# Kernel optimization log

Hardware: AMD Instinct MI355X
Metric: run time of the kernel (lower is better)

Reference implementation:

```python
import jax, jax.numpy as jnp
import numpy as np

N_NODES = 50000
N_EDGES = 800000
F_IN = 128
HID = 128
N_GRAPHS = 512


def setup_inputs() -> dict:
    key = jax.random.key(0)
    k0, k1, k2, k3, k4 = jax.random.split(key, 5)
    x = jax.random.normal(k0, (N_NODES, F_IN), dtype=jnp.float32)
    edge_index = jax.random.randint(k1, (2, N_EDGES), 0, N_NODES)
    batch = jnp.sort(jax.random.randint(k2, (N_NODES,), 0, N_GRAPHS))
    W1 = jax.random.normal(k3, (F_IN, HID), dtype=jnp.float32) / np.sqrt(F_IN).astype(np.float32)
    b1 = jnp.zeros((HID,), dtype=jnp.float32)
    W2 = jax.random.normal(k4, (HID, HID), dtype=jnp.float32) / np.sqrt(HID).astype(np.float32)
    b2 = jnp.zeros((HID,), dtype=jnp.float32)
    return {"x": x, "W1": W1, "b1": b1, "W2": W2, "b2": b2,
            "edge_index": edge_index, "batch": batch}


def _gcn_conv(x, W, b, src, dst, norm, n_nodes):
    # PyG GCNConv: linear transform, then D^-1/2 (A+I) D^-1/2 aggregation, then bias
    h = x @ W                              # [N, H]
    msg = h[src] * norm[:, None]           # gather + edgewise scale  [E+N, H]
    out = jax.ops.segment_sum(msg, dst, num_segments=n_nodes)  # scatter-add
    return out + b


def reference(x, W1, b1, W2, b2, edge_index, batch):
    n = x.shape[0]
    loops = jnp.arange(n)
    src = jnp.concatenate([edge_index[0], loops])   # add self-loops
    dst = jnp.concatenate([edge_index[1], loops])
    deg = jax.ops.segment_sum(jnp.ones_like(dst, dtype=x.dtype), dst, num_segments=n)
    dinv = jax.lax.rsqrt(deg)                       # deg >= 1 due to self-loops
    norm = dinv[src] * dinv[dst]

    h = jax.nn.relu(_gcn_conv(x, W1, b1, src, dst, norm, n))
    h = jax.nn.relu(_gcn_conv(h, W2, b2, src, dst, norm, n))

    # readout mode 'all': concat(add, max, mean) pooling over graphs
    s = jax.ops.segment_sum(h, batch, num_segments=N_GRAPHS)        # [G, H]
    cnt = jax.ops.segment_sum(jnp.ones((n, 1), h.dtype), batch, num_segments=N_GRAPHS)
    mean = s / jnp.maximum(cnt, 1.0)
    mx = jax.ops.segment_max(h, batch, num_segments=N_GRAPHS)
    mx = jnp.where(cnt > 0, mx, 0.0)                # guard empty graphs
    # dropout(p=0.2) is identity in eval mode
    return jnp.concatenate([s, mx, mean], axis=1)   # [G, 3*H]
```

## Files before the change

kernel.cpp:

```cpp
#include <hip/hip_runtime.h>

#define N_NODES 50000
#define N_EDGES 800000
#define FEAT 128
#define N_GRAPHS 512

#define SCAN_BLK 256
#define N_SCAN_BLOCKS ((N_NODES + SCAN_BLK - 1) / SCAN_BLK)

__device__ __forceinline__ unsigned int f2bf(float f) {
    unsigned int u = __float_as_uint(f);
    return (u + 0x7fffu + ((u >> 16) & 1u)) >> 16;
}
__device__ __forceinline__ float bf_lo(unsigned int u) { return __uint_as_float(u << 16); }
__device__ __forceinline__ float bf_hi(unsigned int u) { return __uint_as_float(u & 0xffff0000u); }

__global__ __launch_bounds__(256) void count_kernel(const int* __restrict__ dst,
                                                    int* __restrict__ cnt) {
    int e = blockIdx.x * 256 + threadIdx.x;
    if (e < N_EDGES) atomicAdd(&cnt[__builtin_nontemporal_load(dst + e)], 1);
}

__global__ __launch_bounds__(SCAN_BLK) void scan_partial_kernel(const int* __restrict__ cnt,
                                                                int* __restrict__ partial) {
    __shared__ int s[SCAN_BLK];
    int i = blockIdx.x * SCAN_BLK + threadIdx.x;
    s[threadIdx.x] = (i < N_NODES) ? cnt[i] : 0;
    __syncthreads();
#pragma unroll
    for (int off = SCAN_BLK / 2; off > 0; off >>= 1) {
        if (threadIdx.x < off) s[threadIdx.x] += s[threadIdx.x + off];
        __syncthreads();
    }
    if (threadIdx.x == 0) partial[blockIdx.x] = s[0];
}

__global__ __launch_bounds__(SCAN_BLK) void scan_apply_kernel(const int* __restrict__ cnt,
                                                              const int* __restrict__ partial,
                                                              int* __restrict__ rowptr,
                                                              float* __restrict__ dinv) {
    __shared__ int s[SCAN_BLK];
    __shared__ int sbase;
    int t = threadIdx.x;
    int bid = blockIdx.x;

    s[t] = (t < bid) ? partial[t] : 0;
    __syncthreads();
#pragma unroll
    for (int off = SCAN_BLK / 2; off > 0; off >>= 1) {
        if (t < off) s[t] += s[t + off];
        __syncthreads();
    }
    if (t == 0) sbase = s[0];
    __syncthreads();

    int i = bid * SCAN_BLK + t;
    int v = (i < N_NODES) ? cnt[i] : 0;
    s[t] = v;
    __syncthreads();
#pragma unroll
    for (int off = 1; off < SCAN_BLK; off <<= 1) {
        int u = (t >= off) ? s[t - off] : 0;
        __syncthreads();
        s[t] += u;
        __syncthreads();
    }
    if (i < N_NODES) {
        rowptr[i] = sbase + s[t] - v;
        dinv[i] = rsqrtf((float)(v + 1));
    }
    if (bid == 0 && t == 0) rowptr[N_NODES] = N_EDGES;
}

__global__ __launch_bounds__(256) void scatter_kernel(const int* __restrict__ src,
                                                      const int* __restrict__ dst,
                                                      const int* __restrict__ rowptr,
                                                      int* __restrict__ woff,
                                                      unsigned short* __restrict__ csr_src) {
    int e = blockIdx.x * 256 + threadIdx.x;
    if (e >= N_EDGES) return;
    int s = __builtin_nontemporal_load(src + e);
    int d = __builtin_nontemporal_load(dst + e);
    int pos = atomicAdd(&woff[d], 1);
    csr_src[rowptr[d] + pos] = (unsigned short)s;
}

__global__ __launch_bounds__(256) void gemm_kernel(const float* __restrict__ X,
                                                   const float* __restrict__ W,
                                                   const float* __restrict__ dinv,
                                                   unsigned int* __restrict__ G, int M) {
    __shared__ float sX[64][132];
    __shared__ float sW[64][132];
    int tid = threadIdx.x;
    int row0 = blockIdx.x * 64;

#pragma unroll
    for (int it = 0; it < 8; ++it) {
        int idx = tid + it * 256;
        int r = idx >> 5, q = idx & 31;
        int grow = row0 + r;
        float4 v = make_float4(0.f, 0.f, 0.f, 0.f);
        if (grow < M) v = *reinterpret_cast<const float4*>(X + grow * 128 + q * 4);
        *reinterpret_cast<float4*>(&sX[r][q * 4]) = v;
    }

    int tx = tid & 15;
    int ty = tid >> 4;
    float acc[4][8];
#pragma unroll
    for (int i = 0; i < 4; ++i)
#pragma unroll
        for (int j = 0; j < 8; ++j) acc[i][j] = 0.f;

    for (int k0 = 0; k0 < 128; k0 += 64) {
        __syncthreads();
#pragma unroll
        for (int it = 0; it < 8; ++it) {
            int idx = tid + it * 256;
            int r = idx >> 5, q = idx & 31;
            *reinterpret_cast<float4*>(&sW[r][q * 4]) =
                *reinterpret_cast<const float4*>(W + (k0 + r) * 128 + q * 4);
        }
        __syncthreads();
#pragma unroll 16
        for (int k = 0; k < 64; ++k) {
            float xv[4];
#pragma unroll
            for (int ri = 0; ri < 4; ++ri) xv[ri] = sX[ty * 4 + ri][k0 + k];
            float4 w0 = *reinterpret_cast<const float4*>(&sW[k][tx * 4]);
            float4 w1 = *reinterpret_cast<const float4*>(&sW[k][64 + tx * 4]);
            float wv[8] = {w0.x, w0.y, w0.z, w0.w, w1.x, w1.y, w1.z, w1.w};
#pragma unroll
            for (int ri = 0; ri < 4; ++ri)
#pragma unroll
                for (int ci = 0; ci < 8; ++ci) acc[ri][ci] += xv[ri] * wv[ci];
        }
    }
#pragma unroll
    for (int ri = 0; ri < 4; ++ri) {
        int grow = row0 + ty * 4 + ri;
        if (grow >= M) continue;
        float sc = dinv[grow];
        uint2 lo, hi;
        lo.x = f2bf(sc * acc[ri][0]) | (f2bf(sc * acc[ri][1]) << 16);
        lo.y = f2bf(sc * acc[ri][2]) | (f2bf(sc * acc[ri][3]) << 16);
        hi.x = f2bf(sc * acc[ri][4]) | (f2bf(sc * acc[ri][5]) << 16);
        hi.y = f2bf(sc * acc[ri][6]) | (f2bf(sc * acc[ri][7]) << 16);
        *reinterpret_cast<uint2*>(G + grow * 64 + tx * 2) = lo;
        *reinterpret_cast<uint2*>(G + grow * 64 + 32 + tx * 2) = hi;
    }
}

__global__ __launch_bounds__(256) void aggregate_kernel(const uint4* __restrict__ G4,
                                                        const float* __restrict__ dinv,
                                                        const int* __restrict__ rowptr,
                                                        const unsigned short* __restrict__ csr_src,
                                                        const float* __restrict__ bias,
                                                        float* __restrict__ Hout, int n) {
    int tid = threadIdx.x;
    int node = blockIdx.x * 16 + (tid >> 4);
    int lane16 = tid & 15;
    bool active = node < n;

    int start = active ? rowptr[node] : 0;
    int end = active ? rowptr[node + 1] : 0;

    float a[8] = {0.f, 0.f, 0.f, 0.f, 0.f, 0.f, 0.f, 0.f};
    if (active) {
        uint4 u = G4[node * 16 + lane16];
        a[0] += bf_lo(u.x); a[1] += bf_hi(u.x);
        a[2] += bf_lo(u.y); a[3] += bf_hi(u.y);
        a[4] += bf_lo(u.z); a[5] += bf_hi(u.z);
        a[6] += bf_lo(u.w); a[7] += bf_hi(u.w);
    }

#define ACC_ROW(sidx)                                   \
    {                                                   \
        uint4 u = G4[(sidx) * 16 + lane16];             \
        a[0] += bf_lo(u.x); a[1] += bf_hi(u.x);         \
        a[2] += bf_lo(u.y); a[3] += bf_hi(u.y);         \
        a[4] += bf_lo(u.z); a[5] += bf_hi(u.z);         \
        a[6] += bf_lo(u.w); a[7] += bf_hi(u.w);         \
    }

    for (int base = start; base < end; base += 16) {
        int idx = base + lane16;
        int s_l = (idx < end) ? (int)csr_src[idx] : 0;
        int nn = min(16, end - base);
        if (nn == 16) {
#pragma unroll 8
            for (int j = 0; j < 16; ++j) {
                int s = __shfl(s_l, j, 16);
                ACC_ROW(s);
            }
        } else {
#pragma unroll 4
            for (int j = 0; j < nn; ++j) {
                int s = __shfl(s_l, j, 16);
                ACC_ROW(s);
            }
        }
    }
#undef ACC_ROW

    if (active) {
        float di = dinv[node];
        float4 b0 = *reinterpret_cast<const float4*>(bias + lane16 * 8);
        float4 b1 = *reinterpret_cast<const float4*>(bias + lane16 * 8 + 4);
        float4 o0, o1;
        o0.x = fmaxf(di * a[0] + b0.x, 0.f);
        o0.y = fmaxf(di * a[1] + b0.y, 0.f);
        o0.z = fmaxf(di * a[2] + b0.z, 0.f);
        o0.w = fmaxf(di * a[3] + b0.w, 0.f);
        o1.x = fmaxf(di * a[4] + b1.x, 0.f);
        o1.y = fmaxf(di * a[5] + b1.y, 0.f);
        o1.z = fmaxf(di * a[6] + b1.z, 0.f);
        o1.w = fmaxf(di * a[7] + b1.w, 0.f);
        *reinterpret_cast<float4*>(Hout + node * 128 + lane16 * 8) = o0;
        *reinterpret_cast<float4*>(Hout + node * 128 + lane16 * 8 + 4) = o1;
    }
}

__global__ __launch_bounds__(256) void readout_kernel(const float* __restrict__ H,
                                                      const int* __restrict__ batch,
                                                      float* __restrict__ out) {
    int g = blockIdx.x;
    int f = threadIdx.x & 127;
    int half = threadIdx.x >> 7;
    const int n = N_NODES;
    auto lb = [&](int key) {
        int lo = 0, hi = n;
        while (lo < hi) {
            int mid = (lo + hi) >> 1;
            if (batch[mid] < key) lo = mid + 1; else hi = mid;
        }
        return lo;
    };
    int start = lb(g), end = lb(g + 1);
    float sum = 0.f, mx = 0.f;
    for (int i = start + half; i < end; i += 2) {
        float v = H[i * 128 + f];
        sum += v;
        mx = fmaxf(mx, v);
    }
    __shared__ float ssum[256], smax[256];
    ssum[threadIdx.x] = sum;
    smax[threadIdx.x] = mx;
    __syncthreads();
    if (half == 0) {
        sum += ssum[threadIdx.x + 128];
        mx = fmaxf(mx, smax[threadIdx.x + 128]);
        int cntg = end - start;
        float mean = sum / fmaxf((float)cntg, 1.0f);
        out[g * 384 + f] = sum;
        out[g * 384 + 128 + f] = mx;
        out[g * 384 + 256 + f] = mean;
    }
}

extern "C" void kernel_launch(void* const* d_in, const int* in_sizes, int n_in,
                              void* d_out, int out_size, void* d_ws, size_t ws_size,
                              hipStream_t stream) {
    const float* x = (const float*)d_in[0];
    const float* W1 = (const float*)d_in[1];
    const float* b1 = (const float*)d_in[2];
    const float* W2 = (const float*)d_in[3];
    const float* b2 = (const float*)d_in[4];
    const int* ei = (const int*)d_in[5];
    const int* batch = (const int*)d_in[6];
    const int* esrc = ei;
    const int* edst = ei + N_EDGES;
    float* out = (float*)d_out;

    char* ws = (char*)d_ws;
    int* cnt       = (int*)(ws + 0);
    int* woff      = (int*)(ws + 200704);
    int* rowptr    = (int*)(ws + 401408);
    float* dinv    = (float*)(ws + 602112);
    int* partial   = (int*)(ws + 802816);
    unsigned short* csr_src = (unsigned short*)(ws + 804864);
    unsigned int* bufG = (unsigned int*)(ws + 2404864);
    float* bufH    = (float*)(ws + 15204864);

    hipMemsetAsync(cnt, 0, N_NODES * sizeof(int), stream);
    hipMemsetAsync(woff, 0, N_NODES * sizeof(int), stream);

    count_kernel<<<N_EDGES / 256, 256, 0, stream>>>(edst, cnt);
    scan_partial_kernel<<<N_SCAN_BLOCKS, SCAN_BLK, 0, stream>>>(cnt, partial);
    scan_apply_kernel<<<N_SCAN_BLOCKS, SCAN_BLK, 0, stream>>>(cnt, partial, rowptr, dinv);
    scatter_kernel<<<N_EDGES / 256, 256, 0, stream>>>(esrc, edst, rowptr, woff, csr_src);

    int gemm_blocks = (N_NODES + 63) / 64;
    int agg_blocks = (N_NODES + 15) / 16;
    gemm_kernel<<<gemm_blocks, 256, 0, stream>>>(x, W1, dinv, bufG, N_NODES);
    aggregate_kernel<<<agg_blocks, 256, 0, stream>>>((const uint4*)bufG, dinv, rowptr, csr_src, b1, bufH, N_NODES);
    gemm_kernel<<<gemm_blocks, 256, 0, stream>>>(bufH, W2, dinv, bufG, N_NODES);
    aggregate_kernel<<<agg_blocks, 256, 0, stream>>>((const uint4*)bufG, dinv, rowptr, csr_src, b2, bufH, N_NODES);
    readout_kernel<<<N_GRAPHS, 256, 0, stream>>>(bufH, batch, out);
}
```

Baseline: 334.2 us.

## Use bf16 MFMA for node-feature GEMM with pre-transposed bf16 weights

After: 330.8 us. Within noise of the previous version (-1.0%).

```diff
diff --git a/kernel.cpp b/kernel.cpp
--- a/kernel.cpp
+++ b/kernel.cpp
@@ -7,6 +7,10 @@
 
 #define SCAN_BLK 256
 #define N_SCAN_BLOCKS ((N_NODES + SCAN_BLK - 1) / SCAN_BLK)
+#define LDK 136
+
+typedef __attribute__((ext_vector_type(8))) short short8;
+typedef __attribute__((ext_vector_type(4))) float f32x4;
 
 __device__ __forceinline__ unsigned int f2bf(float f) {
     unsigned int u = __float_as_uint(f);
@@ -85,12 +89,23 @@
     csr_src[rowptr[d] + pos] = (unsigned short)s;
 }
 
+__global__ __launch_bounds__(256) void wt_kernel(const float* __restrict__ W,
+                                                 unsigned short* __restrict__ Wt) {
+    int t = threadIdx.x;
+#pragma unroll
+    for (int i = 0; i < 64; ++i) {
+        int idx = t + 256 * i;
+        int k = idx >> 7, n = idx & 127;
+        Wt[n * 128 + k] = (unsigned short)f2bf(W[idx]);
+    }
+}
+
 __global__ __launch_bounds__(256) void gemm_kernel(const float* __restrict__ X,
-                                                   const float* __restrict__ W,
+                                                   const unsigned short* __restrict__ Wt,
                                                    const float* __restrict__ dinv,
-                                                   unsigned int* __restrict__ G, int M) {
-    __shared__ float sX[64][132];
-    __shared__ float sW[64][132];
+                                                   unsigned short* __restrict__ G16, int M) {
+    __shared__ unsigned short sX[64][LDK];
+    __shared__ unsigned short sW[128][LDK];
     int tid = threadIdx.x;
     int row0 = blockIdx.x * 64;
 
@@ -101,53 +116,51 @@
         int grow = row0 + r;
         float4 v = make_float4(0.f, 0.f, 0.f, 0.f);
         if (grow < M) v = *reinterpret_cast<const float4*>(X + grow * 128 + q * 4);
-        *reinterpret_cast<float4*>(&sX[r][q * 4]) = v;
-    }
-
-    int tx = tid & 15;
-    int ty = tid >> 4;
-    float acc[4][8];
-#pragma unroll
-    for (int i = 0; i < 4; ++i)
-#pragma unroll
-        for (int j = 0; j < 8; ++j) acc[i][j] = 0.f;
-
-    for (int k0 = 0; k0 < 128; k0 += 64) {
-        __syncthreads();
-#pragma unroll
-        for (int it = 0; it < 8; ++it) {
-            int idx = tid + it * 256;
-            int r = idx >> 5, q = idx & 31;
-            *reinterpret_cast<float4*>(&sW[r][q * 4]) =
-                *reinterpret_cast<const float4*>(W + (k0 + r) * 128 + q * 4);
+        uint2 pk;
+        pk.x = f2bf(v.x) | (f2bf(v.y) << 16);
+        pk.y = f2bf(v.z) | (f2bf(v.w) << 16);
+        *reinterpret_cast<uint2*>(&sX[r][q * 4]) = pk;
+    }
+#pragma unroll
+    for (int it = 0; it < 16; ++it) {
+        int idx = tid + it * 256;
+        int n = idx >> 5, q = idx & 31;
+        uint2 v = *reinterpret_cast<const uint2*>(Wt + n * 128 + q * 4);
+        *reinterpret_cast<uint2*>(&sW[n][q * 4]) = v;
+    }
+    __syncthreads();
+
+    int lane = tid & 63;
+    int w = tid >> 6;
+    int r = lane & 15;
+    int g = lane >> 4;
+
+    short8 av[4];
+#pragma unroll
+    for (int g2 = 0; g2 < 4; ++g2)
+        av[g2] = *reinterpret_cast<const short8*>(&sX[16 * w + r][g2 * 32 + g * 8]);
+
+    float dv[4];
+    int gr[4];
+#pragma unroll
+    for (int reg = 0; reg < 4; ++reg) {
+        gr[reg] = row0 + 16 * w + 4 * g + reg;
+        dv[reg] = (gr[reg] < M) ? dinv[gr[reg]] : 0.f;
+    }
+
+#pragma unroll
+    for (int nb = 0; nb < 8; ++nb) {
+        f32x4 c = {0.f, 0.f, 0.f, 0.f};
+#pragma unroll
+        for (int g2 = 0; g2 < 4; ++g2) {
+            short8 bv = *reinterpret_cast<const short8*>(&sW[nb * 16 + r][g2 * 32 + g * 8]);
+            c = __builtin_amdgcn_mfma_f32_16x16x32_bf16(av[g2], bv, c, 0, 0, 0);
         }
-        __syncthreads();
-#pragma unroll 16
-        for (int k = 0; k < 64; ++k) {
-            float xv[4];
-#pragma unroll
-            for (int ri = 0; ri < 4; ++ri) xv[ri] = sX[ty * 4 + ri][k0 + k];
-            float4 w0 = *reinterpret_cast<const float4*>(&sW[k][tx * 4]);
-            float4 w1 = *reinterpret_cast<const float4*>(&sW[k][64 + tx * 4]);
-            float wv[8] = {w0.x, w0.y, w0.z, w0.w, w1.x, w1.y, w1.z, w1.w};
-#pragma unroll
-            for (int ri = 0; ri < 4; ++ri)
-#pragma unroll
-                for (int ci = 0; ci < 8; ++ci) acc[ri][ci] += xv[ri] * wv[ci];
+#pragma unroll
+        for (int reg = 0; reg < 4; ++reg) {
+            if (gr[reg] < M)
+                G16[gr[reg] * 128 + nb * 16 + r] = (unsigned short)f2bf(dv[reg] * c[reg]);
         }
-    }
-#pragma unroll
-    for (int ri = 0; ri < 4; ++ri) {
-        int grow = row0 + ty * 4 + ri;
-        if (grow >= M) continue;
-        float sc = dinv[grow];
-        uint2 lo, hi;
-        lo.x = f2bf(sc * acc[ri][0]) | (f2bf(sc * acc[ri][1]) << 16);
-        lo.y = f2bf(sc * acc[ri][2]) | (f2bf(sc * acc[ri][3]) << 16);
-        hi.x = f2bf(sc * acc[ri][4]) | (f2bf(sc * acc[ri][5]) << 16);
-        hi.y = f2bf(sc * acc[ri][6]) | (f2bf(sc * acc[ri][7]) << 16);
-        *reinterpret_cast<uint2*>(G + grow * 64 + tx * 2) = lo;
-        *reinterpret_cast<uint2*>(G + grow * 64 + 32 + tx * 2) = hi;
     }
 }
 
@@ -279,8 +292,10 @@
     float* dinv    = (float*)(ws + 602112);
     int* partial   = (int*)(ws + 802816);
     unsigned short* csr_src = (unsigned short*)(ws + 804864);
-    unsigned int* bufG = (unsigned int*)(ws + 2404864);
+    unsigned short* bufG = (unsigned short*)(ws + 2404864);
     float* bufH    = (float*)(ws + 15204864);
+    unsigned short* wt1 = (unsigned short*)(ws + 40804864);
+    unsigned short* wt2 = (unsigned short*)(ws + 40837632);
 
     hipMemsetAsync(cnt, 0, N_NODES * sizeof(int), stream);
     hipMemsetAsync(woff, 0, N_NODES * sizeof(int), stream);
@@ -289,12 +304,14 @@
     scan_partial_kernel<<<N_SCAN_BLOCKS, SCAN_BLK, 0, stream>>>(cnt, partial);
     scan_apply_kernel<<<N_SCAN_BLOCKS, SCAN_BLK, 0, stream>>>(cnt, partial, rowptr, dinv);
     scatter_kernel<<<N_EDGES / 256, 256, 0, stream>>>(esrc, edst, rowptr, woff, csr_src);
+    wt_kernel<<<1, 256, 0, stream>>>(W1, wt1);
+    wt_kernel<<<1, 256, 0, stream>>>(W2, wt2);
 
     int gemm_blocks = (N_NODES + 63) / 64;
     int agg_blocks = (N_NODES + 15) / 16;
-    gemm_kernel<<<gemm_blocks, 256, 0, stream>>>(x, W1, dinv, bufG, N_NODES);
+    gemm_kernel<<<gemm_blocks, 256, 0, stream>>>(x, wt1, dinv, bufG, N_NODES);
     aggregate_kernel<<<agg_blocks, 256, 0, stream>>>((const uint4*)bufG, dinv, rowptr, csr_src, b1, bufH, N_NODES);
-    gemm_kernel<<<gemm_blocks, 256, 0, stream>>>(bufH, W2, dinv, bufG, N_NODES);
+    gemm_kernel<<<gemm_blocks, 256, 0, stream>>>(bufH, wt2, dinv, bufG, N_NODES);
     aggregate_kernel<<<agg_blocks, 256, 0, stream>>>((const uint4*)bufG, dinv, rowptr, csr_src, b2, bufH, N_NODES);
     readout_kernel<<<N_GRAPHS, 256, 0, stream>>>(bufH, batch, out);
 }
```
